# Performance work log

Hardware: AMD Instinct MI355X
Metric: run time of the kernel (lower is better)

Reference implementation:

```python
import jax, jax.numpy as jnp
import numpy as np
from functools import partial

N_NODES = 50000
N_EDGES = 800000
IN_F, HID_F, OUT_F = 128, 128, 64


def _linear_params(key, in_f, out_f):
    k1, k2 = jax.random.split(key)
    bound = 1.0 / np.sqrt(in_f)
    W = jax.random.uniform(k1, (out_f, in_f), jnp.float32, -bound, bound)
    b = jax.random.uniform(k2, (out_f,), jnp.float32, -bound, bound)
    return W, b


def setup_inputs() -> dict:
    key = jax.random.key(0)
    ks = jax.random.split(key, 10)
    features = jax.random.normal(ks[0], (N_NODES, IN_F), jnp.float32)
    src = jax.random.randint(ks[1], (N_EDGES,), 0, N_NODES, jnp.int32)
    dst = jax.random.randint(ks[2], (N_EDGES,), 0, N_NODES, jnp.int32)
    W1a, b1a = _linear_params(ks[3], IN_F, HID_F)
    W1b, b1b = _linear_params(ks[4], HID_F, HID_F)
    W2a, b2a = _linear_params(ks[5], HID_F, HID_F)
    W2b, b2b = _linear_params(ks[6], HID_F, HID_F)
    W3a, b3a = _linear_params(ks[7], HID_F, HID_F)
    W3b, b3b = _linear_params(ks[8], HID_F, OUT_F)
    return dict(features=features, src=src, dst=dst,
                W1a=W1a, b1a=b1a, W1b=W1b, b1b=b1b,
                W2a=W2a, b2a=b2a, W2b=W2b, b2b=b2b,
                W3a=W3a, b3a=b3a, W3b=W3b, b3b=b3b)


def _mean_agg(x, src, dst, n_nodes):
    # gather src features, segment-sum into dst, divide by in-degree (0-deg -> 0)
    summed = jax.ops.segment_sum(x[src], dst, num_segments=n_nodes)
    deg = jax.ops.segment_sum(jnp.ones((src.shape[0],), x.dtype), dst,
                              num_segments=n_nodes)
    return summed / jnp.maximum(deg, 1.0)[:, None]


def _gin_conv(x, src, dst, Wa, ba, Wb, bb):
    # DGL GINConv, aggregator 'mean', eps=0: h = MLP((1+eps)*x + mean_agg)
    h = x + _mean_agg(x, src, dst, x.shape[0])
    h = jax.nn.relu(h @ Wa.T + ba)
    return h @ Wb.T + bb


def reference(features, src, dst,
              W1a, b1a, W1b, b1b,
              W2a, b2a, W2b, b2b,
              W3a, b3a, W3b, b3b):
    x = jax.nn.relu(_gin_conv(features, src, dst, W1a, b1a, W1b, b1b))
    x = jax.nn.relu(_gin_conv(x, src, dst, W2a, b2a, W2b, b2b))
    x = jax.nn.relu(x @ W3a.T + b3a)
    return x @ W3b.T + b3b
```

## Files before the change

### kernel.cpp

```cpp
#include <hip/hip_runtime.h>
#include <hip/hip_fp16.h>

#define N_NODES 50000
#define N_EDGES 800000

typedef __attribute__((ext_vector_type(8))) short bf16x8;
typedef __attribute__((ext_vector_type(4))) float f32x4;

#define OFF_BUFA   0UL
#define OFF_T16    25600000UL
#define OFF_CNT    38400000UL
#define OFF_W      38600064UL
#define OFF_CSR    38960512UL

#define NB_EDGE 3125
#define NB_W    352
#define NB_FEAT 6250

__device__ __forceinline__ unsigned short bf16_rne(float f) {
  unsigned u = __float_as_uint(f);
  unsigned r = (u + 0x7FFFu + ((u >> 16) & 1u)) >> 16;
  return (unsigned short)r;
}

__device__ __forceinline__ int swz(int row, int b) {
  return (row * 256 + b) ^ ((row & 7) << 4);
}

__global__ __launch_bounds__(256)
void prep_kernel(const int* __restrict__ src, const int* __restrict__ dst,
                 int* __restrict__ cnt, int* __restrict__ csr,
                 const float* __restrict__ W1a, const float* __restrict__ W1b,
                 const float* __restrict__ W2a, const float* __restrict__ W2b,
                 const float* __restrict__ W3a, const float* __restrict__ W3b,
                 unsigned short* __restrict__ pool,
                 const float* __restrict__ feat, __half* __restrict__ t16) {
  const int b = blockIdx.x;
  const int tid = threadIdx.x;
  if (b < NB_EDGE) {
    int i = b * 256 + tid;
    int d = dst[i];
    int pos = atomicAdd(&cnt[d], 1);
    if (pos < 64) csr[(d << 6) + pos] = src[i];
  } else if (b < NB_EDGE + NB_W) {
    int i = (b - NB_EDGE) * 256 + tid;
    const float* s;
    int base, local, msize;
    if (i < 16384)      { s = W1a; base = 0;      local = i;          msize = 16384; }
    else if (i < 32768) { s = W1b; base = 32768;  local = i - 16384;  msize = 16384; }
    else if (i < 49152) { s = W2a; base = 65536;  local = i - 32768;  msize = 16384; }
    else if (i < 65536) { s = W2b; base = 98304;  local = i - 49152;  msize = 16384; }
    else if (i < 81920) { s = W3a; base = 131072; local = i - 65536;  msize = 16384; }
    else                { s = W3b; base = 163840; local = i - 81920;  msize = 8192;  }
    float f = s[local];
    unsigned short hi = bf16_rne(f);
    float fh = __uint_as_float((unsigned)hi << 16);
    pool[base + local] = hi;
    pool[base + msize + local] = bf16_rne(f - fh);
  } else {
    int i = (b - NB_EDGE - NB_W) * 1024 + tid * 4;
    float4 v = *reinterpret_cast<const float4*>(feat + i);
    ushort4 h;
    h.x = __half_as_ushort(__float2half_rn(v.x));
    h.y = __half_as_ushort(__float2half_rn(v.y));
    h.z = __half_as_ushort(__float2half_rn(v.z));
    h.w = __half_as_ushort(__float2half_rn(v.w));
    *reinterpret_cast<ushort4*>((unsigned short*)t16 + i) = h;
  }
}

template <bool SELF32>
__global__ __launch_bounds__(256)
void agg_kernel(const __half* __restrict__ t16, const float* __restrict__ xself,
                const int* __restrict__ csr, const int* __restrict__ cnt,
                float* __restrict__ out) {
  int node = blockIdx.x * 4 + (threadIdx.x >> 6);
  if (node >= N_NODES) return;
  const int lane = threadIdx.x & 63;
  int deg = cnt[node];
  int dloop = min(deg, 64);
  int beg = node << 6;
  float inv = 1.0f / fmaxf((float)deg, 1.0f);

  float s0 = 0.f, s1 = 0.f, t0 = 0.f, t1 = 0.f;
  float u0 = 0.f, u1 = 0.f, v0 = 0.f, v1 = 0.f;
  int e = 0;
  for (; e + 3 < dloop; e += 4) {
    int i0 = csr[beg + e], i1 = csr[beg + e + 1], i2 = csr[beg + e + 2], i3 = csr[beg + e + 3];
    float2 a = __half22float2(*reinterpret_cast<const __half2*>(t16 + (size_t)i0 * 128 + lane * 2));
    float2 b = __half22float2(*reinterpret_cast<const __half2*>(t16 + (size_t)i1 * 128 + lane * 2));
    float2 c = __half22float2(*reinterpret_cast<const __half2*>(t16 + (size_t)i2 * 128 + lane * 2));
    float2 d = __half22float2(*reinterpret_cast<const __half2*>(t16 + (size_t)i3 * 128 + lane * 2));
    s0 += a.x; s1 += a.y; t0 += b.x; t1 += b.y;
    u0 += c.x; u1 += c.y; v0 += d.x; v1 += d.y;
  }
  for (; e < dloop; ++e) {
    int i0 = csr[beg + e];
    float2 a = __half22float2(*reinterpret_cast<const __half2*>(t16 + (size_t)i0 * 128 + lane * 2));
    s0 += a.x; s1 += a.y;
  }
  float2 sm = make_float2(s0 + t0 + u0 + v0, s1 + t1 + u1 + v1);
  float2 xv;
  if (SELF32) {
    xv = *reinterpret_cast<const float2*>(xself + (size_t)node * 128 + lane * 2);
  } else {
    xv = __half22float2(*reinterpret_cast<const __half2*>(t16 + (size_t)node * 128 + lane * 2));
  }
  float2 o = make_float2(fmaf(sm.x, inv, xv.x), fmaf(sm.y, inv, xv.y));
  *reinterpret_cast<float2*>(out + (size_t)node * 128 + lane * 2) = o;
}

__device__ __forceinline__ void stage_x(const float* __restrict__ X, int m0, int tid,
                                        char* ahi, char* alo, int M) {
  #pragma unroll
  for (int it = 0; it < 8; ++it) {
    int f = tid + it * 256;
    int row = f >> 5, c = f & 31;
    float4 v = make_float4(0.f, 0.f, 0.f, 0.f);
    if (m0 + row < M)
      v = *reinterpret_cast<const float4*>(X + (size_t)(m0 + row) * 128 + c * 4);
    ushort4 hi, lo;
    float fh;
    hi.x = bf16_rne(v.x); fh = __uint_as_float((unsigned)hi.x << 16); lo.x = bf16_rne(v.x - fh);
    hi.y = bf16_rne(v.y); fh = __uint_as_float((unsigned)hi.y << 16); lo.y = bf16_rne(v.y - fh);
    hi.z = bf16_rne(v.z); fh = __uint_as_float((unsigned)hi.z << 16); lo.z = bf16_rne(v.z - fh);
    hi.w = bf16_rne(v.w); fh = __uint_as_float((unsigned)hi.w << 16); lo.w = bf16_rne(v.w - fh);
    int bo = swz(row, c * 8);
    *reinterpret_cast<ushort4*>(ahi + bo) = hi;
    *reinterpret_cast<ushort4*>(alo + bo) = lo;
  }
}

template <int NB>
__device__ __forceinline__ void load_bfrag(const unsigned short* __restrict__ Wh,
                                           const unsigned short* __restrict__ Wl,
                                           int w, int lrow, int lg,
                                           bf16x8 (&bh)[NB][4], bf16x8 (&bl)[NB][4]) {
  #pragma unroll
  for (int nb = 0; nb < NB; ++nb) {
    int col = w * (16 * NB) + nb * 16 + lrow;
    #pragma unroll
    for (int kk = 0; kk < 4; ++kk) {
      int idx = col * 128 + kk * 32 + lg * 8;
      bh[nb][kk] = *reinterpret_cast<const bf16x8*>(Wh + idx);
      bl[nb][kk] = *reinterpret_cast<const bf16x8*>(Wl + idx);
    }
  }
}

template <int NB>
__device__ __forceinline__ void gemm_lds(const char* ahi, const char* alo, int lrow, int lg,
                                         const bf16x8 (&bh)[NB][4], const bf16x8 (&bl)[NB][4],
                                         f32x4 (&acc)[4][NB]) {
  #pragma unroll
  for (int i = 0; i < 4; ++i)
    #pragma unroll
    for (int nb = 0; nb < NB; ++nb) acc[i][nb] = (f32x4){0.f, 0.f, 0.f, 0.f};
  #pragma unroll
  for (int i = 0; i < 4; ++i) {
    #pragma unroll
    for (int kk = 0; kk < 4; ++kk) {
      int bo = swz(i * 16 + lrow, kk * 64 + lg * 16);
      bf16x8 ah = *reinterpret_cast<const bf16x8*>(ahi + bo);
      bf16x8 al = *reinterpret_cast<const bf16x8*>(alo + bo);
      #pragma unroll
      for (int nb = 0; nb < NB; ++nb) {
        acc[i][nb] = __builtin_amdgcn_mfma_f32_16x16x32_bf16(ah, bh[nb][kk], acc[i][nb], 0, 0, 0);
        acc[i][nb] = __builtin_amdgcn_mfma_f32_16x16x32_bf16(al, bh[nb][kk], acc[i][nb], 0, 0, 0);
        acc[i][nb] = __builtin_amdgcn_mfma_f32_16x16x32_bf16(ah, bl[nb][kk], acc[i][nb], 0, 0, 0);
      }
    }
  }
}

__device__ __forceinline__ void store_h(char* ahi, char* alo, const float* __restrict__ bias,
                                        int w, int lrow, int lg, f32x4 (&acc)[4][2]) {
  #pragma unroll
  for (int i = 0; i < 4; ++i) {
    #pragma unroll
    for (int nb = 0; nb < 2; ++nb) {
      int col = w * 32 + nb * 16 + lrow;
      float b = bias[col];
      #pragma unroll
      for (int r = 0; r < 4; ++r) {
        float v = fmaxf(acc[i][nb][r] + b, 0.f);
        int row = i * 16 + lg * 4 + r;
        unsigned short h = bf16_rne(v);
        float fh = __uint_as_float((unsigned)h << 16);
        unsigned short l2 = bf16_rne(v - fh);
        int bo = swz(row, col * 2);
        *reinterpret_cast<unsigned short*>(ahi + bo) = h;
        *reinterpret_cast<unsigned short*>(alo + bo) = l2;
      }
    }
  }
}

__global__ __launch_bounds__(256)
void mlp1_kernel(const float* __restrict__ X, const unsigned short* __restrict__ p,
                 const float* __restrict__ b1a, const float* __restrict__ b1b,
                 __half* __restrict__ Y, int M) {
  __shared__ unsigned short Ahi[64 * 128];
  __shared__ unsigned short Alo[64 * 128];
  char* ahi = (char*)Ahi;
  char* alo = (char*)Alo;
  const int tid = threadIdx.x;
  const int w = tid >> 6, l = tid & 63;
  const int lrow = l & 15, lg = l >> 4;
  const int m0 = blockIdx.x * 64;

  stage_x(X, m0, tid, ahi, alo, M);
  __syncthreads();

  f32x4 acc[4][2];
  {
    bf16x8 bh[2][4], bl[2][4];
    load_bfrag<2>(p + 0, p + 16384, w, lrow, lg, bh, bl);
    gemm_lds<2>(ahi, alo, lrow, lg, bh, bl, acc);
  }
  __syncthreads();
  {
    bf16x8 bh[2][4], bl[2][4];
    load_bfrag<2>(p + 32768, p + 49152, w, lrow, lg, bh, bl);
    store_h(ahi, alo, b1a, w, lrow, lg, acc);
    __syncthreads();
    gemm_lds<2>(ahi, alo, lrow, lg, bh, bl, acc);
  }
  #pragma unroll
  for (int i = 0; i < 4; ++i) {
    #pragma unroll
    for (int nb = 0; nb < 2; ++nb) {
      int col = w * 32 + nb * 16 + lrow;
      float b = b1b[col];
      #pragma unroll
      for (int r = 0; r < 4; ++r) {
        float v = fmaxf(acc[i][nb][r] + b, 0.f);
        int row = m0 + i * 16 + lg * 4 + r;
        if (row < M) Y[(size_t)row * 128 + col] = __float2half_rn(v);
      }
    }
  }
}

__global__ __launch_bounds__(256)
void mlp2head_kernel(const float* __restrict__ X, const unsigned short* __restrict__ p,
                     const float* __restrict__ b2a, const float* __restrict__ b2b,
                     const float* __restrict__ b3a, const float* __restrict__ b3b,
                     float* __restrict__ Y, int M) {
  __shared__ unsigned short Ahi[64 * 128];
  __shared__ unsigned short Alo[64 * 128];
  char* ahi = (char*)Ahi;
  char* alo = (char*)Alo;
  const int tid = threadIdx.x;
  const int w = tid >> 6, l = tid & 63;
  const int lrow = l & 15, lg = l >> 4;
  const int m0 = blockIdx.x * 64;

  stage_x(X, m0, tid, ahi, alo, M);
  __syncthreads();

  f32x4 acc[4][2];
  {
    bf16x8 bh[2][4], bl[2][4];
    load_bfrag<2>(p + 65536, p + 81920, w, lrow, lg, bh, bl);
    gemm_lds<2>(ahi, alo, lrow, lg, bh, bl, acc);
  }
  __syncthreads();
  {
    bf16x8 bh[2][4], bl[2][4];
    load_bfrag<2>(p + 98304, p + 114688, w, lrow, lg, bh, bl);
    store_h(ahi, alo, b2a, w, lrow, lg, acc);
    __syncthreads();
    gemm_lds<2>(ahi, alo, lrow, lg, bh, bl, acc);
  }
  __syncthreads();
  {
    bf16x8 bh[2][4], bl[2][4];
    load_bfrag<2>(p + 131072, p + 147456, w, lrow, lg, bh, bl);
    store_h(ahi, alo, b2b, w, lrow, lg, acc);
    __syncthreads();
    gemm_lds<2>(ahi, alo, lrow, lg, bh, bl, acc);
  }
  __syncthreads();
  f32x4 acc1[4][1];
  {
    bf16x8 bh[1][4], bl[1][4];
    load_bfrag<1>(p + 163840, p + 172032, w, lrow, lg, bh, bl);
    store_h(ahi, alo, b3a, w, lrow, lg, acc);
    __syncthreads();
    gemm_lds<1>(ahi, alo, lrow, lg, bh, bl, acc1);
  }
  #pragma unroll
  for (int i = 0; i < 4; ++i) {
    int col = w * 16 + lrow;
    float b = b3b[col];
    #pragma unroll
    for (int r = 0; r < 4; ++r) {
      float v = acc1[i][0][r] + b;
      int row = m0 + i * 16 + lg * 4 + r;
      if (row < M) Y[(size_t)row * 64 + col] = v;
    }
  }
}

extern "C" void kernel_launch(void* const* d_in, const int* in_sizes, int n_in,
                              void* d_out, int out_size, void* d_ws, size_t ws_size,
                              hipStream_t stream) {
  const float* feat = (const float*)d_in[0];
  const int*   esrc = (const int*)d_in[1];
  const int*   edst = (const int*)d_in[2];
  const float* W1a = (const float*)d_in[3];  const float* b1a = (const float*)d_in[4];
  const float* W1b = (const float*)d_in[5];  const float* b1b = (const float*)d_in[6];
  const float* W2a = (const float*)d_in[7];  const float* b2a = (const float*)d_in[8];
  const float* W2b = (const float*)d_in[9];  const float* b2b = (const float*)d_in[10];
  const float* W3a = (const float*)d_in[11]; const float* b3a = (const float*)d_in[12];
  const float* W3b = (const float*)d_in[13]; const float* b3b = (const float*)d_in[14];

  char* ws = (char*)d_ws;
  float*  bufA = (float*)(ws + OFF_BUFA);
  __half* t16  = (__half*)(ws + OFF_T16);
  int*    cnt  = (int*)(ws + OFF_CNT);
  unsigned short* p = (unsigned short*)(ws + OFF_W);
  int*    csr  = (int*)(ws + OFF_CSR);

  hipMemsetAsync(cnt, 0, 200000, stream);

  prep_kernel<<<NB_EDGE + NB_W + NB_FEAT, 256, 0, stream>>>(
      esrc, edst, cnt, csr, W1a, W1b, W2a, W2b, W3a, W3b, p, feat, t16);

  const int AB = (N_NODES + 3) / 4;
  const int GB = (N_NODES + 63) / 64;

  agg_kernel<true><<<AB, 256, 0, stream>>>(t16, feat, csr, cnt, bufA);
  mlp1_kernel<<<GB, 256, 0, stream>>>(bufA, p, b1a, b1b, t16, N_NODES);

  agg_kernel<false><<<AB, 256, 0, stream>>>(t16, feat, csr, cnt, bufA);
  mlp2head_kernel<<<GB, 256, 0, stream>>>(bufA, p, b2a, b2b, b3a, b3b,
                                          (float*)d_out, N_NODES);
}
```

Baseline: 212.4 us.

## Use 16-bit CSR indices, split prep kernel, and halve MLP row tiles

Stores neighbor indices as unsigned short, which halves CSR memory traffic and lets the aggregation loop fetch four indices with one vector load. The fused prep kernel is split into a separate edge-scatter kernel and a weight/feature conversion kernel. The MLP kernels now process 32 rows per block instead of 64, doubling the grid and halving LDS use per block. Node ids up to 50000 fit in 16 bits, so the narrower indices hold only for graphs with fewer than 65536 nodes, and the smaller tiles reload the weight fragments twice as often overall.

```diff
diff --git a/kernel.cpp b/kernel.cpp
--- a/kernel.cpp
+++ b/kernel.cpp
@@ -28,22 +28,24 @@
 }
 
 __global__ __launch_bounds__(256)
-void prep_kernel(const int* __restrict__ src, const int* __restrict__ dst,
-                 int* __restrict__ cnt, int* __restrict__ csr,
-                 const float* __restrict__ W1a, const float* __restrict__ W1b,
+void scatter16(const int* __restrict__ src, const int* __restrict__ dst,
+               int* __restrict__ cnt, unsigned short* __restrict__ csr) {
+  int i = blockIdx.x * 256 + threadIdx.x;
+  int d = dst[i];
+  int pos = atomicAdd(&cnt[d], 1);
+  if (pos < 64) csr[(d << 6) + pos] = (unsigned short)src[i];
+}
+
+__global__ __launch_bounds__(256)
+void conv_kernel(const float* __restrict__ W1a, const float* __restrict__ W1b,
                  const float* __restrict__ W2a, const float* __restrict__ W2b,
                  const float* __restrict__ W3a, const float* __restrict__ W3b,
                  unsigned short* __restrict__ pool,
                  const float* __restrict__ feat, __half* __restrict__ t16) {
   const int b = blockIdx.x;
   const int tid = threadIdx.x;
-  if (b < NB_EDGE) {
+  if (b < NB_W) {
     int i = b * 256 + tid;
-    int d = dst[i];
-    int pos = atomicAdd(&cnt[d], 1);
-    if (pos < 64) csr[(d << 6) + pos] = src[i];
-  } else if (b < NB_EDGE + NB_W) {
-    int i = (b - NB_EDGE) * 256 + tid;
     const float* s;
     int base, local, msize;
     if (i < 16384)      { s = W1a; base = 0;      local = i;          msize = 16384; }
@@ -58,7 +60,7 @@
     pool[base + local] = hi;
     pool[base + msize + local] = bf16_rne(f - fh);
   } else {
-    int i = (b - NB_EDGE - NB_W) * 1024 + tid * 4;
+    int i = (b - NB_W) * 1024 + tid * 4;
     float4 v = *reinterpret_cast<const float4*>(feat + i);
     ushort4 h;
     h.x = __half_as_ushort(__float2half_rn(v.x));
@@ -72,7 +74,7 @@
 template <bool SELF32>
 __global__ __launch_bounds__(256)
 void agg_kernel(const __half* __restrict__ t16, const float* __restrict__ xself,
-                const int* __restrict__ csr, const int* __restrict__ cnt,
+                const unsigned short* __restrict__ csr, const int* __restrict__ cnt,
                 float* __restrict__ out) {
   int node = blockIdx.x * 4 + (threadIdx.x >> 6);
   if (node >= N_NODES) return;
@@ -86,11 +88,11 @@
   float u0 = 0.f, u1 = 0.f, v0 = 0.f, v1 = 0.f;
   int e = 0;
   for (; e + 3 < dloop; e += 4) {
-    int i0 = csr[beg + e], i1 = csr[beg + e + 1], i2 = csr[beg + e + 2], i3 = csr[beg + e + 3];
-    float2 a = __half22float2(*reinterpret_cast<const __half2*>(t16 + (size_t)i0 * 128 + lane * 2));
-    float2 b = __half22float2(*reinterpret_cast<const __half2*>(t16 + (size_t)i1 * 128 + lane * 2));
-    float2 c = __half22float2(*reinterpret_cast<const __half2*>(t16 + (size_t)i2 * 128 + lane * 2));
-    float2 d = __half22float2(*reinterpret_cast<const __half2*>(t16 + (size_t)i3 * 128 + lane * 2));
+    ushort4 q = *reinterpret_cast<const ushort4*>(csr + beg + e);
+    float2 a = __half22float2(*reinterpret_cast<const __half2*>(t16 + (size_t)q.x * 128 + lane * 2));
+    float2 b = __half22float2(*reinterpret_cast<const __half2*>(t16 + (size_t)q.y * 128 + lane * 2));
+    float2 c = __half22float2(*reinterpret_cast<const __half2*>(t16 + (size_t)q.z * 128 + lane * 2));
+    float2 d = __half22float2(*reinterpret_cast<const __half2*>(t16 + (size_t)q.w * 128 + lane * 2));
     s0 += a.x; s1 += a.y; t0 += b.x; t1 += b.y;
     u0 += c.x; u1 += c.y; v0 += d.x; v1 += d.y;
   }
@@ -110,10 +112,10 @@
   *reinterpret_cast<float2*>(out + (size_t)node * 128 + lane * 2) = o;
 }
 
-__device__ __forceinline__ void stage_x(const float* __restrict__ X, int m0, int tid,
-                                        char* ahi, char* alo, int M) {
-  #pragma unroll
-  for (int it = 0; it < 8; ++it) {
+__device__ __forceinline__ void stage_x32(const float* __restrict__ X, int m0, int tid,
+                                          char* ahi, char* alo, int M) {
+  #pragma unroll
+  for (int it = 0; it < 4; ++it) {
     int f = tid + it * 256;
     int row = f >> 5, c = f & 31;
     float4 v = make_float4(0.f, 0.f, 0.f, 0.f);
@@ -149,15 +151,15 @@
 }
 
 template <int NB>
-__device__ __forceinline__ void gemm_lds(const char* ahi, const char* alo, int lrow, int lg,
-                                         const bf16x8 (&bh)[NB][4], const bf16x8 (&bl)[NB][4],
-                                         f32x4 (&acc)[4][NB]) {
-  #pragma unroll
-  for (int i = 0; i < 4; ++i)
+__device__ __forceinline__ void gemm_lds32(const char* ahi, const char* alo, int lrow, int lg,
+                                           const bf16x8 (&bh)[NB][4], const bf16x8 (&bl)[NB][4],
+                                           f32x4 (&acc)[2][NB]) {
+  #pragma unroll
+  for (int i = 0; i < 2; ++i)
     #pragma unroll
     for (int nb = 0; nb < NB; ++nb) acc[i][nb] = (f32x4){0.f, 0.f, 0.f, 0.f};
   #pragma unroll
-  for (int i = 0; i < 4; ++i) {
+  for (int i = 0; i < 2; ++i) {
     #pragma unroll
     for (int kk = 0; kk < 4; ++kk) {
       int bo = swz(i * 16 + lrow, kk * 64 + lg * 16);
@@ -173,10 +175,10 @@
   }
 }
 
-__device__ __forceinline__ void store_h(char* ahi, char* alo, const float* __restrict__ bias,
-                                        int w, int lrow, int lg, f32x4 (&acc)[4][2]) {
-  #pragma unroll
-  for (int i = 0; i < 4; ++i) {
+__device__ __forceinline__ void store_h32(char* ahi, char* alo, const float* __restrict__ bias,
+                                          int w, int lrow, int lg, f32x4 (&acc)[2][2]) {
+  #pragma unroll
+  for (int i = 0; i < 2; ++i) {
     #pragma unroll
     for (int nb = 0; nb < 2; ++nb) {
       int col = w * 32 + nb * 16 + lrow;
@@ -200,34 +202,34 @@
 void mlp1_kernel(const float* __restrict__ X, const unsigned short* __restrict__ p,
                  const float* __restrict__ b1a, const float* __restrict__ b1b,
                  __half* __restrict__ Y, int M) {
-  __shared__ unsigned short Ahi[64 * 128];
-  __shared__ unsigned short Alo[64 * 128];
+  __shared__ unsigned short Ahi[32 * 128];
+  __shared__ unsigned short Alo[32 * 128];
   char* ahi = (char*)Ahi;
   char* alo = (char*)Alo;
   const int tid = threadIdx.x;
   const int w = tid >> 6, l = tid & 63;
   const int lrow = l & 15, lg = l >> 4;
-  const int m0 = blockIdx.x * 64;
-
-  stage_x(X, m0, tid, ahi, alo, M);
-  __syncthreads();
-
-  f32x4 acc[4][2];
+  const int m0 = blockIdx.x * 32;
+
+  stage_x32(X, m0, tid, ahi, alo, M);
+  __syncthreads();
+
+  f32x4 acc[2][2];
   {
     bf16x8 bh[2][4], bl[2][4];
     load_bfrag<2>(p + 0, p + 16384, w, lrow, lg, bh, bl);
-    gemm_lds<2>(ahi, alo, lrow, lg, bh, bl, acc);
+    gemm_lds32<2>(ahi, alo, lrow, lg, bh, bl, acc);
   }
   __syncthreads();
   {
     bf16x8 bh[2][4], bl[2][4];
     load_bfrag<2>(p + 32768, p + 49152, w, lrow, lg, bh, bl);
-    store_h(ahi, alo, b1a, w, lrow, lg, acc);
+    store_h32(ahi, alo, b1a, w, lrow, lg, acc);
     __syncthreads();
-    gemm_lds<2>(ahi, alo, lrow, lg, bh, bl, acc);
-  }
-  #pragma unroll
-  for (int i = 0; i < 4; ++i) {
+    gemm_lds32<2>(ahi, alo, lrow, lg, bh, bl, acc);
+  }
+  #pragma unroll
+  for (int i = 0; i < 2; ++i) {
     #pragma unroll
     for (int nb = 0; nb < 2; ++nb) {
       int col = w * 32 + nb * 16 + lrow;
@@ -247,51 +249,51 @@
                      const float* __restrict__ b2a, const float* __restrict__ b2b,
                      const float* __restrict__ b3a, const float* __restrict__ b3b,
                      float* __restrict__ Y, int M) {
-  __shared__ unsigned short Ahi[64 * 128];
-  __shared__ unsigned short Alo[64 * 128];
+  __shared__ unsigned short Ahi[32 * 128];
+  __shared__ unsigned short Alo[32 * 128];
   char* ahi = (char*)Ahi;
   char* alo = (char*)Alo;
   const int tid = threadIdx.x;
   const int w = tid >> 6, l = tid & 63;
   const int lrow = l & 15, lg = l >> 4;
-  const int m0 = blockIdx.x * 64;
-
-  stage_x(X, m0, tid, ahi, alo, M);
-  __syncthreads();
-
-  f32x4 acc[4][2];
+  const int m0 = blockIdx.x * 32;
+
+  stage_x32(X, m0, tid, ahi, alo, M);
+  __syncthreads();
+
+  f32x4 acc[2][2];
   {
     bf16x8 bh[2][4], bl[2][4];
     load_bfrag<2>(p + 65536, p + 81920, w, lrow, lg, bh, bl);
-    gemm_lds<2>(ahi, alo, lrow, lg, bh, bl, acc);
+    gemm_lds32<2>(ahi, alo, lrow, lg, bh, bl, acc);
   }
   __syncthreads();
   {
     bf16x8 bh[2][4], bl[2][4];
     load_bfrag<2>(p + 98304, p + 114688, w, lrow, lg, bh, bl);
-    store_h(ahi, alo, b2a, w, lrow, lg, acc);
+    store_h32(ahi, alo, b2a, w, lrow, lg, acc);
     __syncthreads();
-    gemm_lds<2>(ahi, alo, lrow, lg, bh, bl, acc);
+    gemm_lds32<2>(ahi, alo, lrow, lg, bh, bl, acc);
   }
   __syncthreads();
   {
     bf16x8 bh[2][4], bl[2][4];
     load_bfrag<2>(p + 131072, p + 147456, w, lrow, lg, bh, bl);
-    store_h(ahi, alo, b2b, w, lrow, lg, acc);
+    store_h32(ahi, alo, b2b, w, lrow, lg, acc);
     __syncthreads();
-    gemm_lds<2>(ahi, alo, lrow, lg, bh, bl, acc);
-  }
-  __syncthreads();
-  f32x4 acc1[4][1];
+    gemm_lds32<2>(ahi, alo, lrow, lg, bh, bl, acc);
+  }
+  __syncthreads();
+  f32x4 acc1[2][1];
   {
     bf16x8 bh[1][4], bl[1][4];
     load_bfrag<1>(p + 163840, p + 172032, w, lrow, lg, bh, bl);
-    store_h(ahi, alo, b3a, w, lrow, lg, acc);
+    store_h32(ahi, alo, b3a, w, lrow, lg, acc);
     __syncthreads();
-    gemm_lds<1>(ahi, alo, lrow, lg, bh, bl, acc1);
-  }
-  #pragma unroll
-  for (int i = 0; i < 4; ++i) {
+    gemm_lds32<1>(ahi, alo, lrow, lg, bh, bl, acc1);
+  }
+  #pragma unroll
+  for (int i = 0; i < 2; ++i) {
     int col = w * 16 + lrow;
     float b = b3b[col];
     #pragma unroll
@@ -320,16 +322,16 @@
   float*  bufA = (float*)(ws + OFF_BUFA);
   __half* t16  = (__half*)(ws + OFF_T16);
   int*    cnt  = (int*)(ws + OFF_CNT);
-  unsigned short* p = (unsigned short*)(ws + OFF_W);
-  int*    csr  = (int*)(ws + OFF_CSR);
+  unsigned short* p   = (unsigned short*)(ws + OFF_W);
+  unsigned short* csr = (unsigned short*)(ws + OFF_CSR);
 
   hipMemsetAsync(cnt, 0, 200000, stream);
 
-  prep_kernel<<<NB_EDGE + NB_W + NB_FEAT, 256, 0, stream>>>(
-      esrc, edst, cnt, csr, W1a, W1b, W2a, W2b, W3a, W3b, p, feat, t16);
+  scatter16<<<NB_EDGE, 256, 0, stream>>>(esrc, edst, cnt, csr);
+  conv_kernel<<<NB_W + NB_FEAT, 256, 0, stream>>>(W1a, W1b, W2a, W2b, W3a, W3b, p, feat, t16);
 
   const int AB = (N_NODES + 3) / 4;
-  const int GB = (N_NODES + 63) / 64;
+  const int GB = (N_NODES + 31) / 32;
 
   agg_kernel<true><<<AB, 256, 0, stream>>>(t16, feat, csr, cnt, bufA);
   mlp1_kernel<<<GB, 256, 0, stream>>>(bufA, p, b1a, b1b, t16, N_NODES);
```

New measurement: 224.3 us. +5.6%, slower.
